# Optimization experiments

Measured on AMD Instinct MI355X. Metric: run time of the kernel, lower is better.

The kernel has to match this reference:

```python
import jax, jax.numpy as jnp
import numpy as np

N = 50000          # nodes
E = 600000         # edges
D_IN = 256         # input_feat_dim
H1 = 128           # hidden_dim1
H2 = 64            # hidden_dim2
DK = 64            # trs_depth (total key/value depth)
HEADS = 2


def setup_inputs() -> dict:
    key = jax.random.key(0)
    ks = jax.random.split(key, 12)
    inp = {
        "ns_emb": jax.random.normal(ks[0], (N, D_IN), dtype=jnp.float32),
        "edge_rows": jax.random.randint(ks[1], (E,), 0, N, dtype=jnp.int32),
        "edge_cols": jax.random.randint(ks[2], (E,), 0, N, dtype=jnp.int32),
        "edge_vals": jax.random.uniform(ks[3], (E,), dtype=jnp.float32),
        "condition": jax.random.normal(ks[4], (1, 128, H1), dtype=jnp.float32),
        # GCN linear weights (bias=False), stored [in, out]
        "W_hidden": jax.random.normal(ks[5], (D_IN, H1), dtype=jnp.float32) / np.sqrt(D_IN),
        "W_mu": jax.random.normal(ks[6], (H1, H2), dtype=jnp.float32) / np.sqrt(H1),
        "W_var": jax.random.normal(ks[7], (H1, H2), dtype=jnp.float32) / np.sqrt(H1),
        # MultiHeadAttention (bias-free) projections
        "Wq": jax.random.normal(ks[8], (H1, DK), dtype=jnp.float32) / np.sqrt(H1),
        "Wk": jax.random.normal(ks[9], (H1, DK), dtype=jnp.float32) / np.sqrt(H1),
        "Wv": jax.random.normal(ks[10], (H1, DK), dtype=jnp.float32) / np.sqrt(H1),
        "Wo": jax.random.normal(ks[11], (DK, H1), dtype=jnp.float32) / np.sqrt(DK),
    }
    return inp


def _spmm(rows, cols, vals, x):
    # sparse [N,N] @ x  via gather + segment-sum over COO edges
    gathered = vals[:, None] * x[cols]            # [E, d]
    return jax.ops.segment_sum(gathered, rows, num_segments=N)


def _gcn(x, W, rows, cols, vals):
    # dropout is identity in eval mode
    support = jax.nn.leaky_relu(x @ W)            # [N, out]
    out = _spmm(rows, cols, vals, support)        # [N, out]
    return jax.nn.leaky_relu(out)


def _mha(q, kv, Wq, Wk, Wv, Wo):
    # MoEL-style MultiHeadAttention, bias-free, no mask/dropout
    B, Lq, _ = q.shape
    Lk = kv.shape[1]
    dk = DK // HEADS
    Q = (q @ Wq).reshape(B, Lq, HEADS, dk).transpose(0, 2, 1, 3) * (dk ** -0.5)
    K = (kv @ Wk).reshape(B, Lk, HEADS, dk).transpose(0, 2, 1, 3)
    V = (kv @ Wv).reshape(B, Lk, HEADS, dk).transpose(0, 2, 1, 3)
    logits = jnp.einsum("bhqd,bhkd->bhqk", Q, K)
    w = jax.nn.softmax(logits, axis=-1)
    ctx = jnp.einsum("bhqk,bhkd->bhqd", w, V)
    ctx = ctx.transpose(0, 2, 1, 3).reshape(B, Lq, DK)
    return ctx @ Wo, w


def reference(ns_emb, edge_rows, edge_cols, edge_vals, condition,
              W_hidden, W_mu, W_var, Wq, Wk, Wv, Wo):
    hidden = _gcn(ns_emb, W_hidden, edge_rows, edge_cols, edge_vals)   # [N, H1]
    attended, _ = _mha(hidden[None], condition, Wq, Wk, Wv, Wo)        # [1, N, H1]
    h = attended[0]
    mu = _gcn(h, W_mu, edge_rows, edge_cols, edge_vals)                # [N, H2]
    var = _gcn(h, W_var, edge_rows, edge_cols, edge_vals)              # [N, H2]
    return mu, var
```

## Files before the change

### kernel.cpp

```cpp
#include <hip/hip_runtime.h>
#include <hip/hip_bf16.h>
#include <cstdint>


typedef __attribute__((ext_vector_type(8))) short short8;
typedef __attribute__((ext_vector_type(4))) float f32x4;
typedef __attribute__((ext_vector_type(4))) unsigned short ushort4_t;

__device__ __forceinline__ unsigned short f2bf(float f) {
    unsigned int u = __builtin_bit_cast(unsigned int, f);
    u += 0x7fffu + ((u >> 16) & 1u);
    return (unsigned short)(u >> 16);
}
__device__ __forceinline__ float bf2f(unsigned short v) {
    return __builtin_bit_cast(float, (unsigned int)v << 16);
}
__device__ __forceinline__ unsigned int pk2(float a, float b) {
    unsigned int r;
    asm("v_cvt_pk_bf16_f32 %0, %1, %2" : "=v"(r) : "v"(a), "v"(b));
    return r;
}


__global__ void hist_kernel(const int* __restrict__ rows, int* __restrict__ cnt, int E) {
    int i = blockIdx.x * blockDim.x + threadIdx.x;
    if (i < E) atomicAdd(&cnt[rows[i]], 1);
}

__global__ void scan1_kernel(const int* __restrict__ cnt, int* __restrict__ excl,
                             int* __restrict__ bsum, int N) {
    __shared__ int sh[256];
    int t = threadIdx.x;
    int i = blockIdx.x * 256 + t;
    int v = (i < N) ? cnt[i] : 0;
    sh[t] = v;
    __syncthreads();
    for (int off = 1; off < 256; off <<= 1) {
        int x = (t >= off) ? sh[t - off] : 0;
        __syncthreads();
        sh[t] += x;
        __syncthreads();
    }
    if (i < N) excl[i] = sh[t] - v;
    if (t == 255) bsum[blockIdx.x] = sh[255];
}

__global__ void scan23_kernel(const int* __restrict__ excl, const int* __restrict__ bsum,
                              int* __restrict__ row_start, int* __restrict__ cursor,
                              int nb, int N, int E) {
    __shared__ int sh[256];
    int t = threadIdx.x;
    int v = (t < nb) ? bsum[t] : 0;
    sh[t] = v;
    __syncthreads();
    for (int off = 1; off < 256; off <<= 1) {
        int x = (t >= off) ? sh[t - off] : 0;
        __syncthreads();
        sh[t] += x;
        __syncthreads();
    }
    int boff = (blockIdx.x > 0) ? sh[blockIdx.x - 1] : 0;
    int i = blockIdx.x * 256 + t;
    if (i < N) {
        int w = excl[i] + boff;
        row_start[i] = w;
        cursor[i] = w;
    }
    if (i == 0) row_start[N] = E;
}

__global__ void scatter_kernel(const int* __restrict__ rows, const int* __restrict__ colsIn,
                               const float* __restrict__ valsIn, int* __restrict__ cursor,
                               int2* __restrict__ pack, int E) {
    int i = blockIdx.x * blockDim.x + threadIdx.x;
    if (i < E) {
        int r = rows[i];
        int p = atomicAdd(&cursor[r], 1);
        pack[p] = make_int2(colsIn[i], __float_as_int(valsIn[i]));
    }
}


__global__ __launch_bounds__(256) void prep_kv_kernel(
    const float* __restrict__ Wh, const float* __restrict__ Wq,
    const float* __restrict__ cond,
    const float* __restrict__ Wk, const float* __restrict__ Wv,
    const float* __restrict__ Wo, const float* __restrict__ Wmu,
    const float* __restrict__ Wvar,
    unsigned short* __restrict__ WhT, unsigned short* __restrict__ WqT,
    unsigned short* __restrict__ Ktt, unsigned short* __restrict__ Vt,
    unsigned short* __restrict__ WomT)
{
    const int t = threadIdx.x;
    const int bid = blockIdx.x;
    if (bid < 160) {
        int idx = bid * 256 + t;
        if (idx < 32768) {
            int n = idx & 127, k = idx >> 7;
            WhT[n * 256 + k] = f2bf(Wh[k * 128 + n]);
        } else {
            int i = idx - 32768, n = i & 63, k = i >> 6;
            WqT[n * 128 + k] = f2bf(Wq[k * 64 + n]);
        }
    } else if (bid < 224) {
        int b2 = bid - 160;
        __shared__ float c[2][128];
        c[t >> 7][t & 127] = cond[b2 * 256 + t];
        __syncthreads();
        int j = b2 * 2 + (t >> 7);
        int tl = t & 127;
        const float* W = (tl < 64) ? Wk : Wv;
        int col = tl & 63;
        float acc = 0.f;
#pragma unroll 8
        for (int k = 0; k < 128; ++k) acc = fmaf(c[t >> 7][k], W[k * 64 + col], acc);
        int h = col >> 5, d = col & 31;
        if (tl < 64) Ktt[((size_t)h * 128 + j) * 32 + d] = f2bf(acc * 0.17677669529663687f);
        else         Vt[((size_t)h * 32 + d) * 128 + j] = f2bf(acc);
    } else {
        int wb = bid - 224;
        __shared__ float WoTl[128 * 65];
#pragma unroll
        for (int i = 0; i < 32; ++i) {
            int idx = t + 256 * i;
            int d = idx >> 7, k = idx & 127;
            WoTl[k * 65 + d] = Wo[idx];
        }
        __syncthreads();
        int o = wb * 256 + t;
        int d = o & 63, n = o >> 6;
        const float* W = (n < 64) ? Wmu : Wvar;
        int j = n & 63;
        float acc = 0.f;
#pragma unroll 8
        for (int k = 0; k < 128; ++k) acc = fmaf(WoTl[k * 65 + d], W[k * 64 + j], acc);
        WomT[n * 64 + d] = f2bf(acc);
    }
}


__global__ __launch_bounds__(256) void gcn1_gemm(
    const float* __restrict__ A, const unsigned short* __restrict__ BT,
    unsigned short* __restrict__ C, int M)
{
    __shared__ unsigned short As[128][72];
    __shared__ unsigned short Bs[128][72];

    const int tid = threadIdx.x;
    const int lane = tid & 63, wave = tid >> 6;
    const int wm = wave & 1, wn = wave >> 1;
    const int quad = lane >> 4, l16 = lane & 15;
    const int r0 = blockIdx.x * 128;

    f32x4 acc[4][4];
#pragma unroll
    for (int mt = 0; mt < 4; ++mt)
#pragma unroll
        for (int nt = 0; nt < 4; ++nt)
#pragma unroll
            for (int r = 0; r < 4; ++r) acc[mt][nt][r] = 0.f;

    for (int kc = 0; kc < 256; kc += 64) {
#pragma unroll
        for (int i = 0; i < 8; ++i) {
            int f = tid + 256 * i;
            int row = f >> 4, kq = (f & 15) << 2;
            int gr = r0 + row;
            if (gr >= M) gr = M - 1;
            float4 v = *reinterpret_cast<const float4*>(&A[(size_t)gr * 256 + kc + kq]);
            unsigned int lo = pk2(v.x, v.y), hi = pk2(v.z, v.w);
            *reinterpret_cast<uint2*>(&As[row][kq]) = make_uint2(lo, hi);
        }
#pragma unroll
        for (int i = 0; i < 4; ++i) {
            int f = tid + 256 * i;
            int n = f >> 3, k8 = (f & 7) << 3;
            *reinterpret_cast<short8*>(&Bs[n][k8]) =
                *reinterpret_cast<const short8*>(&BT[(size_t)n * 256 + kc + k8]);
        }
        __syncthreads();

#pragma unroll
        for (int ks = 0; ks < 2; ++ks) {
            const int koff = ks * 32 + quad * 8;
            short8 a[4], b[4];
#pragma unroll
            for (int mt = 0; mt < 4; ++mt)
                a[mt] = *reinterpret_cast<const short8*>(&As[wm * 64 + mt * 16 + l16][koff]);
#pragma unroll
            for (int nt = 0; nt < 4; ++nt)
                b[nt] = *reinterpret_cast<const short8*>(&Bs[wn * 64 + nt * 16 + l16][koff]);
#pragma unroll
            for (int mt = 0; mt < 4; ++mt)
#pragma unroll
                for (int nt = 0; nt < 4; ++nt)
                    acc[mt][nt] = __builtin_amdgcn_mfma_f32_16x16x32_bf16(
                        a[mt], b[nt], acc[mt][nt], 0, 0, 0);
        }
        __syncthreads();
    }

#pragma unroll
    for (int mt = 0; mt < 4; ++mt)
#pragma unroll
        for (int nt = 0; nt < 4; ++nt) {
            int gc = wn * 64 + nt * 16 + l16;
#pragma unroll
            for (int r = 0; r < 4; ++r) {
                int gr = r0 + wm * 64 + mt * 16 + quad * 4 + r;
                if (gr < M) {
                    float v = acc[mt][nt][r];
                    v = v > 0.f ? v : 0.01f * v;
                    C[(size_t)gr * 128 + gc] = f2bf(v);
                }
            }
        }
}


__global__ __launch_bounds__(256) void attn_muvar_kernel(
    const unsigned short* __restrict__ hidden,
    const unsigned short* __restrict__ WqT,
    const unsigned short* __restrict__ Ktt,
    const unsigned short* __restrict__ Vt,
    const unsigned short* __restrict__ WomT,
    unsigned short* __restrict__ muvar,
    int M)
{
    __shared__ unsigned short Qs[4][16 * 72];
    __shared__ unsigned short Ps[4][16 * 136];
    __shared__ unsigned short Csh[4][16 * 72];

    const int tid = threadIdx.x;
    const int lane = tid & 63, wave = tid >> 6;
    const int quad = lane >> 4, l16 = lane & 15;

    const int strip = blockIdx.x * 4 + wave;
    const int base = strip * 16;
    if (base >= M) return;
    int qrow = base + l16;
    if (qrow >= M) qrow = M - 1;

    unsigned short* Q  = &Qs[wave][0];
    unsigned short* P  = &Ps[wave][0];
    unsigned short* Cl = &Csh[wave][0];

    {
        f32x4 qacc[4];
#pragma unroll
        for (int mt = 0; mt < 4; ++mt)
#pragma unroll
            for (int r = 0; r < 4; ++r) qacc[mt][r] = 0.f;

        short8 hb[4];
#pragma unroll
        for (int ks = 0; ks < 4; ++ks)
            hb[ks] = *reinterpret_cast<const short8*>(
                &hidden[(size_t)qrow * 128 + ks * 32 + quad * 8]);
#pragma unroll
        for (int mt = 0; mt < 4; ++mt)
#pragma unroll
            for (int ks = 0; ks < 4; ++ks) {
                short8 a = *reinterpret_cast<const short8*>(
                    &WqT[(size_t)(mt * 16 + l16) * 128 + ks * 32 + quad * 8]);
                qacc[mt] = __builtin_amdgcn_mfma_f32_16x16x32_bf16(a, hb[ks], qacc[mt], 0, 0, 0);
            }
#pragma unroll
        for (int mt = 0; mt < 4; ++mt) {
            uint2 w;
            w.x = pk2(qacc[mt][0], qacc[mt][1]);
            w.y = pk2(qacc[mt][2], qacc[mt][3]);
            *reinterpret_cast<uint2*>(&Q[l16 * 72 + mt * 16 + quad * 4]) = w;
        }
    }

    f32x4 ctv[2][2];
#pragma unroll
    for (int h = 0; h < 2; ++h)
#pragma unroll
        for (int mt = 0; mt < 2; ++mt)
#pragma unroll
            for (int r = 0; r < 4; ++r) ctv[h][mt][r] = 0.f;

#pragma unroll
    for (int h = 0; h < 2; ++h) {
        f32x4 st[8];
        short8 qb = *reinterpret_cast<const short8*>(&Q[l16 * 72 + h * 32 + quad * 8]);
#pragma unroll
        for (int mt = 0; mt < 8; ++mt) {
            short8 a = *reinterpret_cast<const short8*>(
                &Ktt[(size_t)h * 4096 + (mt * 16 + l16) * 32 + quad * 8]);
            f32x4 z; z[0] = 0.f; z[1] = 0.f; z[2] = 0.f; z[3] = 0.f;
            st[mt] = __builtin_amdgcn_mfma_f32_16x16x32_bf16(a, qb, z, 0, 0, 0);
        }

        float mx = st[0][0];
#pragma unroll
        for (int mt = 0; mt < 8; ++mt)
#pragma unroll
            for (int r = 0; r < 4; ++r) mx = fmaxf(mx, st[mt][r]);
        mx = fmaxf(mx, __shfl_xor(mx, 16, 64));
        mx = fmaxf(mx, __shfl_xor(mx, 32, 64));
        float s = 0.f;
#pragma unroll
        for (int mt = 0; mt < 8; ++mt)
#pragma unroll
            for (int r = 0; r < 4; ++r) {
                float e = __expf(st[mt][r] - mx);
                st[mt][r] = e;
                s += e;
            }
        s += __shfl_xor(s, 16, 64);
        s += __shfl_xor(s, 32, 64);
        float inv = 1.0f / s;

#pragma unroll
        for (int mt = 0; mt < 8; ++mt) {
            uint2 w;
            w.x = pk2(st[mt][0] * inv, st[mt][1] * inv);
            w.y = pk2(st[mt][2] * inv, st[mt][3] * inv);
            *reinterpret_cast<uint2*>(&P[l16 * 136 + mt * 16 + quad * 4]) = w;
        }

#pragma unroll
        for (int ks = 0; ks < 4; ++ks) {
            short8 pb = *reinterpret_cast<const short8*>(&P[l16 * 136 + ks * 32 + quad * 8]);
#pragma unroll
            for (int mt = 0; mt < 2; ++mt) {
                short8 a = *reinterpret_cast<const short8*>(
                    &Vt[(size_t)h * 4096 + (mt * 16 + l16) * 128 + ks * 32 + quad * 8]);
                ctv[h][mt] = __builtin_amdgcn_mfma_f32_16x16x32_bf16(a, pb, ctv[h][mt], 0, 0, 0);
            }
        }
    }

#pragma unroll
    for (int h = 0; h < 2; ++h)
#pragma unroll
        for (int mt = 0; mt < 2; ++mt) {
            uint2 w;
            w.x = pk2(ctv[h][mt][0], ctv[h][mt][1]);
            w.y = pk2(ctv[h][mt][2], ctv[h][mt][3]);
            *reinterpret_cast<uint2*>(&Cl[l16 * 72 + h * 32 + mt * 16 + quad * 4]) = w;
        }

    {
        f32x4 mv[8];
#pragma unroll
        for (int mt = 0; mt < 8; ++mt)
#pragma unroll
            for (int r = 0; r < 4; ++r) mv[mt][r] = 0.f;
        short8 cb[2];
#pragma unroll
        for (int ks = 0; ks < 2; ++ks)
            cb[ks] = *reinterpret_cast<const short8*>(&Cl[l16 * 72 + ks * 32 + quad * 8]);
#pragma unroll
        for (int mt = 0; mt < 8; ++mt)
#pragma unroll
            for (int ks = 0; ks < 2; ++ks) {
                short8 a = *reinterpret_cast<const short8*>(
                    &WomT[(size_t)(mt * 16 + l16) * 64 + ks * 32 + quad * 8]);
                mv[mt] = __builtin_amdgcn_mfma_f32_16x16x32_bf16(a, cb[ks], mv[mt], 0, 0, 0);
            }
        if (base + l16 < M) {
#pragma unroll
            for (int mt = 0; mt < 8; ++mt) {
                float v0 = mv[mt][0], v1 = mv[mt][1], v2 = mv[mt][2], v3 = mv[mt][3];
                v0 = v0 > 0.f ? v0 : 0.01f * v0;
                v1 = v1 > 0.f ? v1 : 0.01f * v1;
                v2 = v2 > 0.f ? v2 : 0.01f * v2;
                v3 = v3 > 0.f ? v3 : 0.01f * v3;
                uint2 w;
                w.x = pk2(v0, v1);
                w.y = pk2(v2, v3);
                *reinterpret_cast<uint2*>(
                    &muvar[(size_t)(base + l16) * 128 + mt * 16 + quad * 4]) = w;
            }
        }
    }
}


template<bool SPLIT, typename OT>
__global__ __launch_bounds__(256) void spmm_kernel(
    const int* __restrict__ row_start, const int2* __restrict__ pack,
    const unsigned short* __restrict__ X,
    OT* __restrict__ out0, OT* __restrict__ out1, int N)
{
    const int wave = threadIdx.x >> 6, lane = threadIdx.x & 63;
    const int r = blockIdx.x * 4 + wave;
    if (r >= N) return;
    int s = __builtin_amdgcn_readfirstlane(row_start[r]);
    int e = __builtin_amdgcn_readfirstlane(row_start[r + 1]);
    const int fo = lane * 2;

    float ax[8], ay[8];
#pragma unroll
    for (int k = 0; k < 8; ++k) { ax[k] = 0.f; ay[k] = 0.f; }

    int i = s;
    for (; i + 8 <= e; i += 8) {
        int2 p[8];
        unsigned int x[8];
#pragma unroll
        for (int k = 0; k < 8; ++k) p[k] = pack[i + k];
#pragma unroll
        for (int k = 0; k < 8; ++k)
            x[k] = *reinterpret_cast<const unsigned int*>(&X[(size_t)p[k].x * 128 + fo]);
#pragma unroll
        for (int k = 0; k < 8; ++k) {
            float v = __int_as_float(p[k].y);
            ax[k] = fmaf(v, bf2f((unsigned short)x[k]), ax[k]);
            ay[k] = fmaf(v, bf2f((unsigned short)(x[k] >> 16)), ay[k]);
        }
    }
    if (i < e) {
        int2 p[8];
        unsigned int x[8];
#pragma unroll
        for (int k = 0; k < 8; ++k) {
            int idx = i + k;
            p[k] = pack[idx < e ? idx : e - 1];
        }
#pragma unroll
        for (int k = 0; k < 8; ++k)
            x[k] = *reinterpret_cast<const unsigned int*>(&X[(size_t)p[k].x * 128 + fo]);
#pragma unroll
        for (int k = 0; k < 8; ++k) {
            float v = (i + k < e) ? __int_as_float(p[k].y) : 0.f;
            ax[k] = fmaf(v, bf2f((unsigned short)x[k]), ax[k]);
            ay[k] = fmaf(v, bf2f((unsigned short)(x[k] >> 16)), ay[k]);
        }
    }

    float ox = ((ax[0] + ax[1]) + (ax[2] + ax[3])) + ((ax[4] + ax[5]) + (ax[6] + ax[7]));
    float oy = ((ay[0] + ay[1]) + (ay[2] + ay[3])) + ((ay[4] + ay[5]) + (ay[6] + ay[7]));
    ox = ox > 0.f ? ox : 0.01f * ox;
    oy = oy > 0.f ? oy : 0.01f * oy;

    if constexpr (!SPLIT) {
        unsigned int w = (unsigned int)f2bf(ox) | ((unsigned int)f2bf(oy) << 16);
        *reinterpret_cast<unsigned int*>(&out0[(size_t)r * 128 + fo]) = w;
    } else {
        if (lane < 32) {
            *reinterpret_cast<float2*>(&out0[(size_t)r * 64 + fo]) = make_float2(ox, oy);
        } else {
            *reinterpret_cast<float2*>(&out1[(size_t)r * 64 + (fo - 64)]) = make_float2(ox, oy);
        }
    }
}


extern "C" void kernel_launch(void* const* d_in, const int* in_sizes, int n_in,
                              void* d_out, int out_size, void* d_ws, size_t ws_size,
                              hipStream_t stream)
{
    const float* ns_emb   = (const float*)d_in[0];
    const int*   erows    = (const int*)d_in[1];
    const int*   ecols    = (const int*)d_in[2];
    const float* evals    = (const float*)d_in[3];
    const float* cond     = (const float*)d_in[4];
    const float* W_hidden = (const float*)d_in[5];
    const float* W_mu     = (const float*)d_in[6];
    const float* W_var    = (const float*)d_in[7];
    const float* Wq       = (const float*)d_in[8];
    const float* Wk       = (const float*)d_in[9];
    const float* Wv       = (const float*)d_in[10];
    const float* Wo       = (const float*)d_in[11];

    const int N = in_sizes[0] / 256;
    const int E = in_sizes[1];

    typedef unsigned short bf16;
    uint8_t* p = (uint8_t*)d_ws;
    auto alloc = [&](size_t bytes) {
        uint8_t* r = p;
        p += (bytes + 255) & ~(size_t)255;
        return r;
    };
    bf16* support1 = (bf16*)alloc(sizeof(bf16) * (size_t)N * 128);
    bf16* hidden   = (bf16*)alloc(sizeof(bf16) * (size_t)N * 128);
    bf16* muvarb   = (bf16*)alloc(sizeof(bf16) * (size_t)N * 128);
    bf16* Ktt      = (bf16*)alloc(sizeof(bf16) * 2 * 128 * 32);
    bf16* Vt       = (bf16*)alloc(sizeof(bf16) * 2 * 32 * 128);
    bf16* WhT      = (bf16*)alloc(sizeof(bf16) * 128 * 256);
    bf16* WqT      = (bf16*)alloc(sizeof(bf16) * 64 * 128);
    bf16* WomT     = (bf16*)alloc(sizeof(bf16) * 128 * 64);
    int*  cnt      = (int*)alloc(sizeof(int) * N);
    int*  excl     = (int*)alloc(sizeof(int) * N);
    int*  bsum     = (int*)alloc(sizeof(int) * 256);
    int*  row_start= (int*)alloc(sizeof(int) * (N + 1));
    int*  cursor   = (int*)alloc(sizeof(int) * N);
    int2* pack     = (int2*)alloc(sizeof(int2) * E);

    hipMemsetAsync(cnt, 0, sizeof(int) * N, stream);
    hist_kernel<<<(E + 255) / 256, 256, 0, stream>>>(erows, cnt, E);
    int nb = (N + 255) / 256;
    scan1_kernel<<<nb, 256, 0, stream>>>(cnt, excl, bsum, N);
    scan23_kernel<<<nb, 256, 0, stream>>>(excl, bsum, row_start, cursor, nb, N, E);
    scatter_kernel<<<(E + 255) / 256, 256, 0, stream>>>(erows, ecols, evals, cursor, pack, E);

    prep_kv_kernel<<<256, 256, 0, stream>>>(W_hidden, Wq, cond, Wk, Wv,
                                            Wo, W_mu, W_var,
                                            WhT, WqT, Ktt, Vt, WomT);

    const int mb128 = (N + 127) / 128;
    const int strips = (N + 15) / 16;
    const int ablocks = (strips + 3) / 4;
    const int sblocks = (N + 3) / 4;

    gcn1_gemm<<<mb128, 256, 0, stream>>>(ns_emb, WhT, support1, N);
    spmm_kernel<false, bf16><<<sblocks, 256, 0, stream>>>(
        row_start, pack, support1, hidden, nullptr, N);

    attn_muvar_kernel<<<ablocks, 256, 0, stream>>>(hidden, WqT, Ktt, Vt,
                                                   WomT, muvarb, N);

    float* out = (float*)d_out;
    spmm_kernel<true, float><<<sblocks, 256, 0, stream>>>(
        row_start, pack, muvarb, out, out + (size_t)N * 64, N);
}
```

Before: 270.2 us.

## Fuse first SpMM into attention kernel and merge histogram, prep and scan launches

The first GCN SpMM now runs inside the attention kernel: each block aggregates 16 hidden rows into shared memory, and wave 0 then runs the attention and mu/var projection. This drops the global hidden buffer round-trip and one launch. The histogram is merged into the weight-prep kernel, and the two scan kernels become one decoupled-lookback style scan that spin-waits on per-block flags. In exchange, three of the four waves sit idle during the attention phase, and the spin-wait scan relies on earlier blocks being scheduled before later ones to avoid deadlock.

```diff
diff --git a/kernel.cpp b/kernel.cpp
--- a/kernel.cpp
+++ b/kernel.cpp
@@ -5,7 +5,6 @@
 
 typedef __attribute__((ext_vector_type(8))) short short8;
 typedef __attribute__((ext_vector_type(4))) float f32x4;
-typedef __attribute__((ext_vector_type(4))) unsigned short ushort4_t;
 
 __device__ __forceinline__ unsigned short f2bf(float f) {
     unsigned int u = __builtin_bit_cast(unsigned int, f);
@@ -22,66 +21,8 @@
 }
 
 
-__global__ void hist_kernel(const int* __restrict__ rows, int* __restrict__ cnt, int E) {
-    int i = blockIdx.x * blockDim.x + threadIdx.x;
-    if (i < E) atomicAdd(&cnt[rows[i]], 1);
-}
-
-__global__ void scan1_kernel(const int* __restrict__ cnt, int* __restrict__ excl,
-                             int* __restrict__ bsum, int N) {
-    __shared__ int sh[256];
-    int t = threadIdx.x;
-    int i = blockIdx.x * 256 + t;
-    int v = (i < N) ? cnt[i] : 0;
-    sh[t] = v;
-    __syncthreads();
-    for (int off = 1; off < 256; off <<= 1) {
-        int x = (t >= off) ? sh[t - off] : 0;
-        __syncthreads();
-        sh[t] += x;
-        __syncthreads();
-    }
-    if (i < N) excl[i] = sh[t] - v;
-    if (t == 255) bsum[blockIdx.x] = sh[255];
-}
-
-__global__ void scan23_kernel(const int* __restrict__ excl, const int* __restrict__ bsum,
-                              int* __restrict__ row_start, int* __restrict__ cursor,
-                              int nb, int N, int E) {
-    __shared__ int sh[256];
-    int t = threadIdx.x;
-    int v = (t < nb) ? bsum[t] : 0;
-    sh[t] = v;
-    __syncthreads();
-    for (int off = 1; off < 256; off <<= 1) {
-        int x = (t >= off) ? sh[t - off] : 0;
-        __syncthreads();
-        sh[t] += x;
-        __syncthreads();
-    }
-    int boff = (blockIdx.x > 0) ? sh[blockIdx.x - 1] : 0;
-    int i = blockIdx.x * 256 + t;
-    if (i < N) {
-        int w = excl[i] + boff;
-        row_start[i] = w;
-        cursor[i] = w;
-    }
-    if (i == 0) row_start[N] = E;
-}
-
-__global__ void scatter_kernel(const int* __restrict__ rows, const int* __restrict__ colsIn,
-                               const float* __restrict__ valsIn, int* __restrict__ cursor,
-                               int2* __restrict__ pack, int E) {
-    int i = blockIdx.x * blockDim.x + threadIdx.x;
-    if (i < E) {
-        int r = rows[i];
-        int p = atomicAdd(&cursor[r], 1);
-        pack[p] = make_int2(colsIn[i], __float_as_int(valsIn[i]));
-    }
-}
-
-
-__global__ __launch_bounds__(256) void prep_kv_kernel(
+__global__ __launch_bounds__(256) void hist_prep_kernel(
+    const int* __restrict__ rows, int* __restrict__ cnt, int E, int HB,
     const float* __restrict__ Wh, const float* __restrict__ Wq,
     const float* __restrict__ cond,
     const float* __restrict__ Wk, const float* __restrict__ Wv,
@@ -92,7 +33,12 @@
     unsigned short* __restrict__ WomT)
 {
     const int t = threadIdx.x;
-    const int bid = blockIdx.x;
+    if ((int)blockIdx.x < HB) {
+        int i = blockIdx.x * 256 + t;
+        if (i < E) atomicAdd(&cnt[rows[i]], 1);
+        return;
+    }
+    const int bid = blockIdx.x - HB;
     if (bid < 160) {
         int idx = bid * 256 + t;
         if (idx < 32768) {
@@ -139,6 +85,63 @@
 }
 
 
+__global__ __launch_bounds__(256) void scan_fused_kernel(
+    const int* __restrict__ cnt, int* __restrict__ bsum, int* __restrict__ flag,
+    int* __restrict__ row_start, int* __restrict__ cursor, int N, int E)
+{
+    __shared__ int sh[256];
+    const int t = threadIdx.x, b = blockIdx.x;
+    const int i = b * 256 + t;
+    int v = (i < N) ? cnt[i] : 0;
+    sh[t] = v;
+    __syncthreads();
+    for (int off = 1; off < 256; off <<= 1) {
+        int x = (t >= off) ? sh[t - off] : 0;
+        __syncthreads();
+        sh[t] += x;
+        __syncthreads();
+    }
+    const int incl = sh[t];
+    const int aggregate = sh[255];
+
+    if (t == 255) {
+        __hip_atomic_store(&bsum[b], aggregate, __ATOMIC_RELAXED, __HIP_MEMORY_SCOPE_AGENT);
+        __hip_atomic_store(&flag[b], 1, __ATOMIC_RELEASE, __HIP_MEMORY_SCOPE_AGENT);
+    }
+
+    int acc = 0;
+    if (t < b) {
+        while (__hip_atomic_load(&flag[t], __ATOMIC_ACQUIRE, __HIP_MEMORY_SCOPE_AGENT) == 0) {}
+        acc = __hip_atomic_load(&bsum[t], __ATOMIC_RELAXED, __HIP_MEMORY_SCOPE_AGENT);
+    }
+    __syncthreads();
+    sh[t] = acc;
+    __syncthreads();
+    for (int off = 128; off > 0; off >>= 1) {
+        if (t < off) sh[t] += sh[t + off];
+        __syncthreads();
+    }
+    const int boff = sh[0];
+    if (i < N) {
+        int w = incl - v + boff;
+        row_start[i] = w;
+        cursor[i] = w;
+    }
+    if (b == 0 && t == 0) row_start[N] = E;
+}
+
+__global__ void scatter_kernel(const int* __restrict__ rows, const int* __restrict__ colsIn,
+                               const float* __restrict__ valsIn, int* __restrict__ cursor,
+                               int2* __restrict__ pack, int E) {
+    int i = blockIdx.x * blockDim.x + threadIdx.x;
+    if (i < E) {
+        int r = rows[i];
+        int p = atomicAdd(&cursor[r], 1);
+        pack[p] = make_int2(colsIn[i], __float_as_int(valsIn[i]));
+    }
+}
+
+
 __global__ __launch_bounds__(256) void gcn1_gemm(
     const float* __restrict__ A, const unsigned short* __restrict__ BT,
     unsigned short* __restrict__ C, int M)
@@ -218,8 +221,9 @@
 }
 
 
-__global__ __launch_bounds__(256) void attn_muvar_kernel(
-    const unsigned short* __restrict__ hidden,
+__global__ __launch_bounds__(256) void spmm_attn_kernel(
+    const int* __restrict__ row_start, const int2* __restrict__ pack,
+    const unsigned short* __restrict__ X,
     const unsigned short* __restrict__ WqT,
     const unsigned short* __restrict__ Ktt,
     const unsigned short* __restrict__ Vt,
@@ -227,23 +231,72 @@
     unsigned short* __restrict__ muvar,
     int M)
 {
-    __shared__ unsigned short Qs[4][16 * 72];
-    __shared__ unsigned short Ps[4][16 * 136];
-    __shared__ unsigned short Csh[4][16 * 72];
+    __shared__ unsigned short hid[16][136];
+    __shared__ unsigned short Q[16 * 72];
+    __shared__ unsigned short P[16 * 136];
+    __shared__ unsigned short Cl[16 * 72];
 
     const int tid = threadIdx.x;
     const int lane = tid & 63, wave = tid >> 6;
     const int quad = lane >> 4, l16 = lane & 15;
-
-    const int strip = blockIdx.x * 4 + wave;
-    const int base = strip * 16;
-    if (base >= M) return;
-    int qrow = base + l16;
-    if (qrow >= M) qrow = M - 1;
-
-    unsigned short* Q  = &Qs[wave][0];
-    unsigned short* P  = &Ps[wave][0];
-    unsigned short* Cl = &Csh[wave][0];
+    const int base = blockIdx.x * 16;
+    const int fo = lane * 2;
+
+    for (int rr = 0; rr < 4; ++rr) {
+        const int row = wave * 4 + rr;
+        int r = base + row;
+        if (r >= M) r = M - 1;
+        int s = __builtin_amdgcn_readfirstlane(row_start[r]);
+        int e = __builtin_amdgcn_readfirstlane(row_start[r + 1]);
+
+        float ax[8], ay[8];
+#pragma unroll
+        for (int k = 0; k < 8; ++k) { ax[k] = 0.f; ay[k] = 0.f; }
+
+        int i = s;
+        for (; i + 8 <= e; i += 8) {
+            int2 p[8];
+            unsigned int x[8];
+#pragma unroll
+            for (int k = 0; k < 8; ++k) p[k] = pack[i + k];
+#pragma unroll
+            for (int k = 0; k < 8; ++k)
+                x[k] = *reinterpret_cast<const unsigned int*>(&X[(size_t)p[k].x * 128 + fo]);
+#pragma unroll
+            for (int k = 0; k < 8; ++k) {
+                float v = __int_as_float(p[k].y);
+                ax[k] = fmaf(v, bf2f((unsigned short)x[k]), ax[k]);
+                ay[k] = fmaf(v, bf2f((unsigned short)(x[k] >> 16)), ay[k]);
+            }
+        }
+        if (i < e) {
+            int2 p[8];
+            unsigned int x[8];
+#pragma unroll
+            for (int k = 0; k < 8; ++k) {
+                int idx = i + k;
+                p[k] = pack[idx < e ? idx : e - 1];
+            }
+#pragma unroll
+            for (int k = 0; k < 8; ++k)
+                x[k] = *reinterpret_cast<const unsigned int*>(&X[(size_t)p[k].x * 128 + fo]);
+#pragma unroll
+            for (int k = 0; k < 8; ++k) {
+                float v = (i + k < e) ? __int_as_float(p[k].y) : 0.f;
+                ax[k] = fmaf(v, bf2f((unsigned short)x[k]), ax[k]);
+                ay[k] = fmaf(v, bf2f((unsigned short)(x[k] >> 16)), ay[k]);
+            }
+        }
+
+        float ox = ((ax[0] + ax[1]) + (ax[2] + ax[3])) + ((ax[4] + ax[5]) + (ax[6] + ax[7]));
+        float oy = ((ay[0] + ay[1]) + (ay[2] + ay[3])) + ((ay[4] + ay[5]) + (ay[6] + ay[7]));
+        ox = ox > 0.f ? ox : 0.01f * ox;
+        oy = oy > 0.f ? oy : 0.01f * oy;
+        unsigned int w = (unsigned int)f2bf(ox) | ((unsigned int)f2bf(oy) << 16);
+        *reinterpret_cast<unsigned int*>(&hid[row][fo]) = w;
+    }
+    __syncthreads();
+    if (wave != 0) return;
 
     {
         f32x4 qacc[4];
@@ -255,8 +308,7 @@
         short8 hb[4];
 #pragma unroll
         for (int ks = 0; ks < 4; ++ks)
-            hb[ks] = *reinterpret_cast<const short8*>(
-                &hidden[(size_t)qrow * 128 + ks * 32 + quad * 8]);
+            hb[ks] = *reinterpret_cast<const short8*>(&hid[l16][ks * 32 + quad * 8]);
 #pragma unroll
         for (int mt = 0; mt < 4; ++mt)
 #pragma unroll
@@ -479,7 +531,6 @@
         return r;
     };
     bf16* support1 = (bf16*)alloc(sizeof(bf16) * (size_t)N * 128);
-    bf16* hidden   = (bf16*)alloc(sizeof(bf16) * (size_t)N * 128);
     bf16* muvarb   = (bf16*)alloc(sizeof(bf16) * (size_t)N * 128);
     bf16* Ktt      = (bf16*)alloc(sizeof(bf16) * 2 * 128 * 32);
     bf16* Vt       = (bf16*)alloc(sizeof(bf16) * 2 * 32 * 128);
@@ -487,35 +538,35 @@
     bf16* WqT      = (bf16*)alloc(sizeof(bf16) * 64 * 128);
     bf16* WomT     = (bf16*)alloc(sizeof(bf16) * 128 * 64);
     int*  cnt      = (int*)alloc(sizeof(int) * N);
-    int*  excl     = (int*)alloc(sizeof(int) * N);
+    int*  flag     = (int*)alloc(sizeof(int) * 256);
     int*  bsum     = (int*)alloc(sizeof(int) * 256);
     int*  row_start= (int*)alloc(sizeof(int) * (N + 1));
     int*  cursor   = (int*)alloc(sizeof(int) * N);
     int2* pack     = (int2*)alloc(sizeof(int2) * E);
 
-    hipMemsetAsync(cnt, 0, sizeof(int) * N, stream);
-    hist_kernel<<<(E + 255) / 256, 256, 0, stream>>>(erows, cnt, E);
-    int nb = (N + 255) / 256;
-    scan1_kernel<<<nb, 256, 0, stream>>>(cnt, excl, bsum, N);
-    scan23_kernel<<<nb, 256, 0, stream>>>(excl, bsum, row_start, cursor, nb, N, E);
-    scatter_kernel<<<(E + 255) / 256, 256, 0, stream>>>(erows, ecols, evals, cursor, pack, E);
-
-    prep_kv_kernel<<<256, 256, 0, stream>>>(W_hidden, Wq, cond, Wk, Wv,
-                                            Wo, W_mu, W_var,
-                                            WhT, WqT, Ktt, Vt, WomT);
+    const int HB = (E + 255) / 256;
+    const int nb = (N + 255) / 256;
+
+    size_t zbytes = (size_t)((uint8_t*)flag - (uint8_t*)cnt) + sizeof(int) * 256;
+    hipMemsetAsync(cnt, 0, zbytes, stream);
+
+    hist_prep_kernel<<<HB + 256, 256, 0, stream>>>(erows, cnt, E, HB,
+                                                   W_hidden, Wq, cond, Wk, Wv,
+                                                   Wo, W_mu, W_var,
+                                                   WhT, WqT, Ktt, Vt, WomT);
+
+    scan_fused_kernel<<<nb, 256, 0, stream>>>(cnt, bsum, flag, row_start, cursor, N, E);
+
+    scatter_kernel<<<HB, 256, 0, stream>>>(erows, ecols, evals, cursor, pack, E);
 
     const int mb128 = (N + 127) / 128;
-    const int strips = (N + 15) / 16;
-    const int ablocks = (strips + 3) / 4;
+    gcn1_gemm<<<mb128, 256, 0, stream>>>(ns_emb, WhT, support1, N);
+
+    const int ablocks = (N + 15) / 16;
+    spmm_attn_kernel<<<ablocks, 256, 0, stream>>>(row_start, pack, support1,
+                                                  WqT, Ktt, Vt, WomT, muvarb, N);
+
     const int sblocks = (N + 3) / 4;
-
-    gcn1_gemm<<<mb128, 256, 0, stream>>>(ns_emb, WhT, support1, N);
-    spmm_kernel<false, bf16><<<sblocks, 256, 0, stream>>>(
-        row_start, pack, support1, hidden, nullptr, N);
-
-    attn_muvar_kernel<<<ablocks, 256, 0, stream>>>(hidden, WqT, Ktt, Vt,
-                                                   WomT, muvarb, N);
-
     float* out = (float*)d_out;
     spmm_kernel<true, float><<<sblocks, 256, 0, stream>>>(
         row_start, pack, muvarb, out, out + (size_t)N * 64, N);
```

Result: slower. 275.7 us (+2.0%).

## Fuse CSR build kernels with decoupled-lookback scan and half-wave-per-row SpMM

Applied to the files above, without the earlier changes.

Merges the histogram kernel with weight preparation, and replaces the two-pass scan with one kernel in which each block spins on per-block flags to collect the prefix of earlier block sums. This removes several launches and the excl buffer. The SpMM now gives each row half a wave, with each lane loading 4 bf16 features via 8-byte loads, and prefetches the next 8 edge pack entries while the current gathers accumulate. The flag-based scan assumes all 196 blocks are co-resident or scheduled in order, otherwise blocks could spin forever.

```diff
diff --git a/kernel.cpp b/kernel.cpp
--- a/kernel.cpp
+++ b/kernel.cpp
@@ -5,7 +5,6 @@
 
 typedef __attribute__((ext_vector_type(8))) short short8;
 typedef __attribute__((ext_vector_type(4))) float f32x4;
-typedef __attribute__((ext_vector_type(4))) unsigned short ushort4_t;
 
 __device__ __forceinline__ unsigned short f2bf(float f) {
     unsigned int u = __builtin_bit_cast(unsigned int, f);
@@ -22,66 +21,8 @@
 }
 
 
-__global__ void hist_kernel(const int* __restrict__ rows, int* __restrict__ cnt, int E) {
-    int i = blockIdx.x * blockDim.x + threadIdx.x;
-    if (i < E) atomicAdd(&cnt[rows[i]], 1);
-}
-
-__global__ void scan1_kernel(const int* __restrict__ cnt, int* __restrict__ excl,
-                             int* __restrict__ bsum, int N) {
-    __shared__ int sh[256];
-    int t = threadIdx.x;
-    int i = blockIdx.x * 256 + t;
-    int v = (i < N) ? cnt[i] : 0;
-    sh[t] = v;
-    __syncthreads();
-    for (int off = 1; off < 256; off <<= 1) {
-        int x = (t >= off) ? sh[t - off] : 0;
-        __syncthreads();
-        sh[t] += x;
-        __syncthreads();
-    }
-    if (i < N) excl[i] = sh[t] - v;
-    if (t == 255) bsum[blockIdx.x] = sh[255];
-}
-
-__global__ void scan23_kernel(const int* __restrict__ excl, const int* __restrict__ bsum,
-                              int* __restrict__ row_start, int* __restrict__ cursor,
-                              int nb, int N, int E) {
-    __shared__ int sh[256];
-    int t = threadIdx.x;
-    int v = (t < nb) ? bsum[t] : 0;
-    sh[t] = v;
-    __syncthreads();
-    for (int off = 1; off < 256; off <<= 1) {
-        int x = (t >= off) ? sh[t - off] : 0;
-        __syncthreads();
-        sh[t] += x;
-        __syncthreads();
-    }
-    int boff = (blockIdx.x > 0) ? sh[blockIdx.x - 1] : 0;
-    int i = blockIdx.x * 256 + t;
-    if (i < N) {
-        int w = excl[i] + boff;
-        row_start[i] = w;
-        cursor[i] = w;
-    }
-    if (i == 0) row_start[N] = E;
-}
-
-__global__ void scatter_kernel(const int* __restrict__ rows, const int* __restrict__ colsIn,
-                               const float* __restrict__ valsIn, int* __restrict__ cursor,
-                               int2* __restrict__ pack, int E) {
-    int i = blockIdx.x * blockDim.x + threadIdx.x;
-    if (i < E) {
-        int r = rows[i];
-        int p = atomicAdd(&cursor[r], 1);
-        pack[p] = make_int2(colsIn[i], __float_as_int(valsIn[i]));
-    }
-}
-
-
-__global__ __launch_bounds__(256) void prep_kv_kernel(
+__global__ __launch_bounds__(256) void hist_prep_kernel(
+    const int* __restrict__ rows, int* __restrict__ cnt, int E, int HB,
     const float* __restrict__ Wh, const float* __restrict__ Wq,
     const float* __restrict__ cond,
     const float* __restrict__ Wk, const float* __restrict__ Wv,
@@ -92,7 +33,12 @@
     unsigned short* __restrict__ WomT)
 {
     const int t = threadIdx.x;
-    const int bid = blockIdx.x;
+    if ((int)blockIdx.x < HB) {
+        int i = blockIdx.x * 256 + t;
+        if (i < E) atomicAdd(&cnt[rows[i]], 1);
+        return;
+    }
+    const int bid = blockIdx.x - HB;
     if (bid < 160) {
         int idx = bid * 256 + t;
         if (idx < 32768) {
@@ -139,6 +85,63 @@
 }
 
 
+__global__ __launch_bounds__(256) void scan_fused_kernel(
+    const int* __restrict__ cnt, int* __restrict__ bsum, int* __restrict__ flag,
+    int* __restrict__ row_start, int* __restrict__ cursor, int N, int E)
+{
+    __shared__ int sh[256];
+    const int t = threadIdx.x, b = blockIdx.x;
+    const int i = b * 256 + t;
+    int v = (i < N) ? cnt[i] : 0;
+    sh[t] = v;
+    __syncthreads();
+    for (int off = 1; off < 256; off <<= 1) {
+        int x = (t >= off) ? sh[t - off] : 0;
+        __syncthreads();
+        sh[t] += x;
+        __syncthreads();
+    }
+    const int incl = sh[t];
+    const int aggregate = sh[255];
+
+    if (t == 255) {
+        __hip_atomic_store(&bsum[b], aggregate, __ATOMIC_RELAXED, __HIP_MEMORY_SCOPE_AGENT);
+        __hip_atomic_store(&flag[b], 1, __ATOMIC_RELEASE, __HIP_MEMORY_SCOPE_AGENT);
+    }
+
+    int acc = 0;
+    if (t < b) {
+        while (__hip_atomic_load(&flag[t], __ATOMIC_ACQUIRE, __HIP_MEMORY_SCOPE_AGENT) == 0) {}
+        acc = __hip_atomic_load(&bsum[t], __ATOMIC_RELAXED, __HIP_MEMORY_SCOPE_AGENT);
+    }
+    __syncthreads();
+    sh[t] = acc;
+    __syncthreads();
+    for (int off = 128; off > 0; off >>= 1) {
+        if (t < off) sh[t] += sh[t + off];
+        __syncthreads();
+    }
+    const int boff = sh[0];
+    if (i < N) {
+        int w = incl - v + boff;
+        row_start[i] = w;
+        cursor[i] = w;
+    }
+    if (b == 0 && t == 0) row_start[N] = E;
+}
+
+__global__ void scatter_kernel(const int* __restrict__ rows, const int* __restrict__ colsIn,
+                               const float* __restrict__ valsIn, int* __restrict__ cursor,
+                               int2* __restrict__ pack, int E) {
+    int i = blockIdx.x * blockDim.x + threadIdx.x;
+    if (i < E) {
+        int r = rows[i];
+        int p = atomicAdd(&cursor[r], 1);
+        pack[p] = make_int2(colsIn[i], __float_as_int(valsIn[i]));
+    }
+}
+
+
 __global__ __launch_bounds__(256) void gcn1_gemm(
     const float* __restrict__ A, const unsigned short* __restrict__ BT,
     unsigned short* __restrict__ C, int M)
@@ -388,64 +391,76 @@
     OT* __restrict__ out0, OT* __restrict__ out1, int N)
 {
     const int wave = threadIdx.x >> 6, lane = threadIdx.x & 63;
-    const int r = blockIdx.x * 4 + wave;
-    if (r >= N) return;
-    int s = __builtin_amdgcn_readfirstlane(row_start[r]);
-    int e = __builtin_amdgcn_readfirstlane(row_start[r + 1]);
-    const int fo = lane * 2;
-
-    float ax[8], ay[8];
-#pragma unroll
-    for (int k = 0; k < 8; ++k) { ax[k] = 0.f; ay[k] = 0.f; }
-
-    int i = s;
-    for (; i + 8 <= e; i += 8) {
+    const int l32 = lane & 31, half = lane >> 5;
+    int r = blockIdx.x * 8 + wave * 2 + half;
+    if (r >= N) r = N - 1;
+    const int s = row_start[r];
+    const int e = row_start[r + 1];
+    const int fo = l32 * 4;
+
+    f32x4 acc[8];
+#pragma unroll
+    for (int k = 0; k < 8; ++k) { acc[k][0] = 0.f; acc[k][1] = 0.f; acc[k][2] = 0.f; acc[k][3] = 0.f; }
+
+    if (s < e) {
+        int i = s;
         int2 p[8];
-        unsigned int x[8];
-#pragma unroll
-        for (int k = 0; k < 8; ++k) p[k] = pack[i + k];
-#pragma unroll
-        for (int k = 0; k < 8; ++k)
-            x[k] = *reinterpret_cast<const unsigned int*>(&X[(size_t)p[k].x * 128 + fo]);
-#pragma unroll
-        for (int k = 0; k < 8; ++k) {
-            float v = __int_as_float(p[k].y);
-            ax[k] = fmaf(v, bf2f((unsigned short)x[k]), ax[k]);
-            ay[k] = fmaf(v, bf2f((unsigned short)(x[k] >> 16)), ay[k]);
-        }
-    }
-    if (i < e) {
-        int2 p[8];
-        unsigned int x[8];
 #pragma unroll
         for (int k = 0; k < 8; ++k) {
             int idx = i + k;
             p[k] = pack[idx < e ? idx : e - 1];
         }
-#pragma unroll
-        for (int k = 0; k < 8; ++k)
-            x[k] = *reinterpret_cast<const unsigned int*>(&X[(size_t)p[k].x * 128 + fo]);
-#pragma unroll
-        for (int k = 0; k < 8; ++k) {
-            float v = (i + k < e) ? __int_as_float(p[k].y) : 0.f;
-            ax[k] = fmaf(v, bf2f((unsigned short)x[k]), ax[k]);
-            ay[k] = fmaf(v, bf2f((unsigned short)(x[k] >> 16)), ay[k]);
-        }
-    }
-
-    float ox = ((ax[0] + ax[1]) + (ax[2] + ax[3])) + ((ax[4] + ax[5]) + (ax[6] + ax[7]));
-    float oy = ((ay[0] + ay[1]) + (ay[2] + ay[3])) + ((ay[4] + ay[5]) + (ay[6] + ay[7]));
-    ox = ox > 0.f ? ox : 0.01f * ox;
-    oy = oy > 0.f ? oy : 0.01f * oy;
+        while (i < e) {
+            uint2 x[8];
+#pragma unroll
+            for (int k = 0; k < 8; ++k)
+                x[k] = *reinterpret_cast<const uint2*>(&X[(size_t)p[k].x * 128 + fo]);
+
+            const int inext = i + 8;
+            int2 pn[8];
+            if (inext < e) {
+#pragma unroll
+                for (int k = 0; k < 8; ++k) {
+                    int idx = inext + k;
+                    pn[k] = pack[idx < e ? idx : e - 1];
+                }
+            }
+#pragma unroll
+            for (int k = 0; k < 8; ++k) {
+                float v = (i + k < e) ? __int_as_float(p[k].y) : 0.f;
+                acc[k][0] = fmaf(v, bf2f((unsigned short)(x[k].x)), acc[k][0]);
+                acc[k][1] = fmaf(v, bf2f((unsigned short)(x[k].x >> 16)), acc[k][1]);
+                acc[k][2] = fmaf(v, bf2f((unsigned short)(x[k].y)), acc[k][2]);
+                acc[k][3] = fmaf(v, bf2f((unsigned short)(x[k].y >> 16)), acc[k][3]);
+            }
+            if (inext < e) {
+#pragma unroll
+                for (int k = 0; k < 8; ++k) p[k] = pn[k];
+            }
+            i = inext;
+        }
+    }
+
+    f32x4 o;
+#pragma unroll
+    for (int j = 0; j < 4; ++j)
+        o[j] = ((acc[0][j] + acc[1][j]) + (acc[2][j] + acc[3][j])) +
+               ((acc[4][j] + acc[5][j]) + (acc[6][j] + acc[7][j]));
+#pragma unroll
+    for (int j = 0; j < 4; ++j)
+        o[j] = o[j] > 0.f ? o[j] : 0.01f * o[j];
 
     if constexpr (!SPLIT) {
-        unsigned int w = (unsigned int)f2bf(ox) | ((unsigned int)f2bf(oy) << 16);
-        *reinterpret_cast<unsigned int*>(&out0[(size_t)r * 128 + fo]) = w;
+        uint2 w;
+        w.x = pk2(o[0], o[1]);
+        w.y = pk2(o[2], o[3]);
+        *reinterpret_cast<uint2*>(&out0[(size_t)r * 128 + fo]) = w;
     } else {
-        if (lane < 32) {
-            *reinterpret_cast<float2*>(&out0[(size_t)r * 64 + fo]) = make_float2(ox, oy);
+        float4 w = make_float4(o[0], o[1], o[2], o[3]);
+        if (fo < 64) {
+            *reinterpret_cast<float4*>(&out0[(size_t)r * 64 + fo]) = w;
         } else {
-            *reinterpret_cast<float2*>(&out1[(size_t)r * 64 + (fo - 64)]) = make_float2(ox, oy);
+            *reinterpret_cast<float4*>(&out1[(size_t)r * 64 + (fo - 64)]) = w;
         }
     }
 }
@@ -487,36 +502,40 @@
     bf16* WqT      = (bf16*)alloc(sizeof(bf16) * 64 * 128);
     bf16* WomT     = (bf16*)alloc(sizeof(bf16) * 128 * 64);
     int*  cnt      = (int*)alloc(sizeof(int) * N);
-    int*  excl     = (int*)alloc(sizeof(int) * N);
+    int*  flag     = (int*)alloc(sizeof(int) * 256);
     int*  bsum     = (int*)alloc(sizeof(int) * 256);
     int*  row_start= (int*)alloc(sizeof(int) * (N + 1));
     int*  cursor   = (int*)alloc(sizeof(int) * N);
     int2* pack     = (int2*)alloc(sizeof(int2) * E);
 
-    hipMemsetAsync(cnt, 0, sizeof(int) * N, stream);
-    hist_kernel<<<(E + 255) / 256, 256, 0, stream>>>(erows, cnt, E);
-    int nb = (N + 255) / 256;
-    scan1_kernel<<<nb, 256, 0, stream>>>(cnt, excl, bsum, N);
-    scan23_kernel<<<nb, 256, 0, stream>>>(excl, bsum, row_start, cursor, nb, N, E);
-    scatter_kernel<<<(E + 255) / 256, 256, 0, stream>>>(erows, ecols, evals, cursor, pack, E);
-
-    prep_kv_kernel<<<256, 256, 0, stream>>>(W_hidden, Wq, cond, Wk, Wv,
-                                            Wo, W_mu, W_var,
-                                            WhT, WqT, Ktt, Vt, WomT);
+    const int HB = (E + 255) / 256;
+    const int nb = (N + 255) / 256;
+
+    size_t zbytes = (size_t)((uint8_t*)flag - (uint8_t*)cnt) + sizeof(int) * 256;
+    hipMemsetAsync(cnt, 0, zbytes, stream);
+
+    hist_prep_kernel<<<HB + 256, 256, 0, stream>>>(erows, cnt, E, HB,
+                                                   W_hidden, Wq, cond, Wk, Wv,
+                                                   Wo, W_mu, W_var,
+                                                   WhT, WqT, Ktt, Vt, WomT);
+
+    scan_fused_kernel<<<nb, 256, 0, stream>>>(cnt, bsum, flag, row_start, cursor, N, E);
+
+    scatter_kernel<<<HB, 256, 0, stream>>>(erows, ecols, evals, cursor, pack, E);
 
     const int mb128 = (N + 127) / 128;
+    gcn1_gemm<<<mb128, 256, 0, stream>>>(ns_emb, WhT, support1, N);
+
+    const int spblocks = (N + 7) / 8;
+    spmm_kernel<false, bf16><<<spblocks, 256, 0, stream>>>(
+        row_start, pack, support1, hidden, nullptr, N);
+
     const int strips = (N + 15) / 16;
     const int ablocks = (strips + 3) / 4;
-    const int sblocks = (N + 3) / 4;
-
-    gcn1_gemm<<<mb128, 256, 0, stream>>>(ns_emb, WhT, support1, N);
-    spmm_kernel<false, bf16><<<sblocks, 256, 0, stream>>>(
-        row_start, pack, support1, hidden, nullptr, N);
-
     attn_muvar_kernel<<<ablocks, 256, 0, stream>>>(hidden, WqT, Ktt, Vt,
                                                    WomT, muvarb, N);
 
     float* out = (float*)d_out;
-    spmm_kernel<true, float><<<sblocks, 256, 0, stream>>>(
+    spmm_kernel<true, float><<<spblocks, 256, 0, stream>>>(
         row_start, pack, muvarb, out, out + (size_t)N * 64, N);
 }
```

Result: slower. 295.2 us (+9.2%).
